# Kernel tuning notes

Measured on AMD Instinct MI355X. Metric: run time of the kernel, lower is better.

The kernel has to match this reference:

```python
import jax, jax.numpy as jnp
import numpy as np

B, N, HID, H, DH, NB = 4, 4096, 768, 12, 64, 266
EPS = 1e-4


def softmax_kernel(data, proj, is_query):
    # data: [B,H,N,DH], proj: [NB,DH]. FAVOR+ positive softmax features.
    d = data.shape[-1]
    ratio = proj.shape[0] ** -0.5
    dn = d ** -0.25  # data normalizer
    data_dash = jnp.einsum('bhnd,jd->bhnj', data * dn, proj)  # [B,H,N,NB]
    diag = 0.5 * jnp.sum((data * dn) ** 2, axis=-1, keepdims=True)  # [B,H,N,1]
    if is_query:
        m = jnp.max(data_dash, axis=-1, keepdims=True)
    else:
        m = jnp.max(data_dash, axis=(-1, -2), keepdims=True)
    return ratio * (jnp.exp(data_dash - diag - m) + EPS)


def setup_inputs() -> dict:
    key = jax.random.key(0)
    ks = jax.random.split(key, 8)
    s = HID ** -0.5
    return {
        'hidden_states': jax.random.normal(ks[0], (B, N, HID), jnp.float32),
        'Wq': jax.random.normal(ks[1], (HID, HID), jnp.float32) * s,
        'bq': jnp.zeros((HID,), jnp.float32),
        'Wk': jax.random.normal(ks[2], (HID, HID), jnp.float32) * s,
        'bk': jnp.zeros((HID,), jnp.float32),
        'Wv': jax.random.normal(ks[3], (HID, HID), jnp.float32) * s,
        'bv': jnp.zeros((HID,), jnp.float32),
        'proj': jax.random.normal(ks[4], (NB, DH), jnp.float32),
    }


def reference(hidden_states, Wq, bq, Wk, bk, Wv, bv, proj):
    def heads(x):  # [B,N,HID] -> [B,H,N,DH]
        return x.reshape(B, N, H, DH).transpose(0, 2, 1, 3)

    q = heads(hidden_states @ Wq.T + bq)
    k = heads(hidden_states @ Wk.T + bk)
    v = heads(hidden_states @ Wv.T + bv)

    qp = softmax_kernel(q, proj, True)   # [B,H,N,NB]
    kp = softmax_kernel(k, proj, False)  # [B,H,N,NB]

    # non-causal linear attention: out = q' (k'^T v) / (q' sum_n k')
    k_sum = jnp.sum(kp, axis=2)                               # [B,H,NB]
    d_inv = 1.0 / jnp.einsum('bhnj,bhj->bhn', qp, k_sum)      # [B,H,N]
    ctx = jnp.einsum('bhnj,bhnd->bhjd', kp, v)                # [B,H,NB,DH]
    out = jnp.einsum('bhnj,bhjd->bhnd', qp, ctx) * d_inv[..., None]

    return out.transpose(0, 2, 1, 3).reshape(B, N, HID)
```

## Files before the change

kernel.cpp:

```cpp
#include <hip/hip_runtime.h>
#include <hip/hip_bf16.h>
#include <stdint.h>

#define B_   4
#define N_   4096
#define HID_ 768
#define H_   12
#define DH_  64
#define NB_  266
#define NBP_ 288
#define EPS_ 1e-4f
#define RATIO_ 0.06131393f

typedef unsigned short u16;
typedef __attribute__((ext_vector_type(8))) short short8;
typedef __attribute__((ext_vector_type(4))) float floatx4;

__device__ __forceinline__ u16 f2b(float f) {
  __hip_bfloat16 h = __float2bfloat16(f);
  return *reinterpret_cast<u16*>(&h);
}
__device__ __forceinline__ float b2f(u16 u) {
  union { unsigned u; float f; } x; x.u = ((unsigned)u) << 16; return x.f;
}
__device__ __forceinline__ unsigned fmap(float x) {
  unsigned u = __float_as_uint(x);
  return (u & 0x80000000u) ? ~u : (u | 0x80000000u);
}
__device__ __forceinline__ float funmap(unsigned u) {
  unsigned b = (u & 0x80000000u) ? (u & 0x7FFFFFFFu) : ~u;
  return __uint_as_float(b);
}
__device__ __forceinline__ void gl16(const u16* g, u16* l) {
  __builtin_amdgcn_global_load_lds(
      (const __attribute__((address_space(1))) void*)g,
      (__attribute__((address_space(3))) void*)l, 16, 0, 0);
}

__global__ __launch_bounds__(256) void k_prep(
    const float4* __restrict__ hs, const float4* __restrict__ Wq,
    const float4* __restrict__ Wk, const float4* __restrict__ Wv,
    const float* __restrict__ proj,
    uint2* __restrict__ hsb, uint2* __restrict__ wb3, u16* __restrict__ projb,
    float* __restrict__ Vdz, unsigned* __restrict__ mbuf) {
  int blk = blockIdx.x;
  const int t = threadIdx.x;
  if (blk < 12288) {
    int i = blk * 256 + t;
    float4 v = hs[i];
    union { u16 s[4]; uint2 u; } pk;
    pk.s[0] = f2b(v.x); pk.s[1] = f2b(v.y); pk.s[2] = f2b(v.z); pk.s[3] = f2b(v.w);
    hsb[i] = pk.u;
    return;
  }
  blk -= 12288;
  if (blk < 1728) {
    int i = blk * 256 + t;
    int sel = i / 147456, j = i - sel * 147456;
    const float4* s = (sel == 0) ? Wq : (sel == 1) ? Wk : Wv;
    float4 v = s[j];
    union { u16 s4[4]; uint2 u; } pk;
    pk.s4[0] = f2b(v.x); pk.s4[1] = f2b(v.y); pk.s4[2] = f2b(v.z); pk.s4[3] = f2b(v.w);
    wb3[i] = pk.u;
    return;
  }
  blk -= 1728;
  if (blk < 72) {
    int i = blk * 256 + t;
    int j = i / DH_, d = i - j * DH_;
    float v = (j < NB_) ? proj[j * DH_ + d] * 0.35355339059327373f : 0.f;
    projb[i] = f2b(v);
    return;
  }
  blk -= 72;
  if (blk < 12) {
    int i = blk * 256 + t;
    Vdz[i] = 0.f;
    return;
  }
  if (t < B_ * H_) mbuf[t] = 0u;
}

__global__ __launch_bounds__(256) void k_qkv3(
    const u16* __restrict__ hsb, const u16* __restrict__ wb,
    const float* __restrict__ bq, const float* __restrict__ bk, const float* __restrict__ bv,
    u16* __restrict__ qb, u16* __restrict__ kb, u16* __restrict__ vT,
    float* __restrict__ diagk, float* __restrict__ Vd) {
  __shared__ u16 lds[3 * 8192];
  const int m0 = blockIdx.x * 128;
  const int bn = blockIdx.y;
  const int sel = bn / 6;
  const int or0 = (bn % 6) * 128;
  const u16* W = wb + (size_t)sel * HID_ * HID_;
  const int t = threadIdx.x, lane = t & 63, wv = t >> 6;
  const int lm = lane & 15, lq = lane >> 4;
  const int wr = (wv >> 1) * 64, wc = (wv & 1) * 64;
  const int srow = t >> 2;
  const int scol = ((t & 3) ^ ((t >> 3) & 3)) * 8;
  const u16* gA0 = hsb + (size_t)(m0 + srow) * HID_ + scol;
  const u16* gB0 = W + (size_t)(or0 + srow) * HID_ + scol;
  u16* lb = lds + wv * 512;
  const int slotc = (lq ^ ((lm >> 1) & 3)) * 8;
  const int aoff = (wr + lm) * 32 + slotc;
  const int boff = 4096 + (wc + lm) * 32 + slotc;

  floatx4 acc[4][4];
#pragma unroll
  for (int mt = 0; mt < 4; mt++)
#pragma unroll
    for (int nt = 0; nt < 4; nt++) acc[mt][nt] = (floatx4){0.f, 0.f, 0.f, 0.f};

#define STAGE_QKV(kt)                                            \
  {                                                              \
    const int k0_ = (kt) * 32;                                   \
    u16* l_ = lb + ((kt) % 3) * 8192;                            \
    gl16(gA0 + k0_, l_);                                         \
    gl16(gA0 + 64 * HID_ + k0_, l_ + 2048);                      \
    gl16(gB0 + k0_, l_ + 4096);                                  \
    gl16(gB0 + 64 * HID_ + k0_, l_ + 6144);                      \
  }

  STAGE_QKV(0);
  STAGE_QKV(1);
  asm volatile("s_waitcnt vmcnt(4)" ::: "memory");
  __builtin_amdgcn_s_barrier();

  for (int kt = 0; kt < 24; ++kt) {
    if (kt + 2 < 24) STAGE_QKV(kt + 2);
    const u16* bufA = lds + (kt % 3) * 8192;
    short8 af[4], bf[4];
#pragma unroll
    for (int mt = 0; mt < 4; mt++) af[mt] = *(const short8*)&bufA[aoff + mt * 512];
#pragma unroll
    for (int nt = 0; nt < 4; nt++) bf[nt] = *(const short8*)&bufA[boff + nt * 512];
    __builtin_amdgcn_s_setprio(1);
#pragma unroll
    for (int mt = 0; mt < 4; mt++)
#pragma unroll
      for (int nt = 0; nt < 4; nt++)
        acc[mt][nt] = __builtin_amdgcn_mfma_f32_16x16x32_bf16(af[mt], bf[nt], acc[mt][nt], 0, 0, 0);
    __builtin_amdgcn_s_setprio(0);
    if (kt < 22) asm volatile("s_waitcnt vmcnt(4)" ::: "memory");
    else         asm volatile("s_waitcnt vmcnt(0)" ::: "memory");
    __builtin_amdgcn_s_barrier();
  }
#undef STAGE_QKV

  if (sel == 0) {
#pragma unroll
    for (int nt = 0; nt < 4; nt++) {
      int lc = or0 + wc + nt * 16 + lm;
      float bb = bq[lc];
#pragma unroll
      for (int mt = 0; mt < 4; mt++) {
        int rowb = m0 + wr + mt * 16 + lq * 4;
#pragma unroll
        for (int r = 0; r < 4; r++)
          qb[(size_t)(rowb + r) * HID_ + lc] = f2b(acc[mt][nt][r] + bb);
      }
    }
  } else if (sel == 1) {
    float dsq[4][4];
#pragma unroll
    for (int mt = 0; mt < 4; mt++)
#pragma unroll
      for (int r = 0; r < 4; r++) dsq[mt][r] = 0.f;
#pragma unroll
    for (int nt = 0; nt < 4; nt++) {
      int lc = or0 + wc + nt * 16 + lm;
      float bb = bk[lc];
#pragma unroll
      for (int mt = 0; mt < 4; mt++) {
        int rowb = m0 + wr + mt * 16 + lq * 4;
#pragma unroll
        for (int r = 0; r < 4; r++) {
          u16 hv = f2b(acc[mt][nt][r] + bb);
          kb[(size_t)(rowb + r) * HID_ + lc] = hv;
          float fv = b2f(hv);
          dsq[mt][r] += fv * fv;
        }
      }
    }
    const int bh0 = (m0 >> 12) * H_ + ((or0 + wc) >> 6);
#pragma unroll
    for (int mt = 0; mt < 4; mt++)
#pragma unroll
      for (int r = 0; r < 4; r++) {
        float v = dsq[mt][r];
        v += __shfl_xor(v, 1); v += __shfl_xor(v, 2);
        v += __shfl_xor(v, 4); v += __shfl_xor(v, 8);
        if (lm == 0) {
          int rowb = m0 + wr + mt * 16 + lq * 4 + r;
          diagk[(size_t)bh0 * N_ + (rowb & 4095)] = 0.0625f * v;
        }
      }
  } else {
    const int hh = (or0 + wc) >> 6;
#pragma unroll
    for (int nt = 0; nt < 4; nt++) {
      int lc = or0 + wc + nt * 16 + lm;
      int dv = nt * 16 + lm;
      float bb = bv[lc];
      float vs = 0.f;
#pragma unroll
      for (int mt = 0; mt < 4; mt++) {
        int rowbase = m0 + wr + mt * 16 + lq * 4;
        int b = rowbase >> 12, n = rowbase & 4095;
        union { u16 s[4]; uint2 u; } pk;
#pragma unroll
        for (int r = 0; r < 4; r++) {
          float fv = acc[mt][nt][r] + bb;
          vs += fv;
          pk.s[r] = f2b(fv);
        }
        *(uint2*)(vT + ((size_t)(b * H_ + hh) * DH_ + dv) * N_ + n) = pk.u;
      }
      vs += __shfl_xor(vs, 16);
      vs += __shfl_xor(vs, 32);
      if (lq == 0) atomicAdd(&Vd[((m0 >> 12) * H_ + hh) * DH_ + dv], vs);
    }
  }
}

__global__ __launch_bounds__(256) void k_ctx5(
    const u16* __restrict__ kb, const u16* __restrict__ vT, const u16* __restrict__ projb,
    const float* __restrict__ diagk,
    float* __restrict__ ksumS, float* __restrict__ ctxTf, unsigned* __restrict__ mbuf) {
  __shared__ u16 kpl[32 * 72];
  __shared__ float kred[4][2][16];
  const int orig = blockIdx.x;
  const int lg = (orig & 7) * 54 + (orig >> 3);
  const int bh = lg / 9, jb = lg - bh * 9;
  const int j0 = jb * 32;
  const int b = bh / H_, h = bh - b * H_;
  const int t = threadIdx.x, lane = t & 63, wv = t >> 6;
  const int lm = lane & 15, lq = lane >> 4;
  const bool vj0 = (j0 + lm) < NB_;
  const bool vj1 = (j0 + 16 + lm) < NB_;
  short8 bp00, bp01, bp10, bp11;
  {
    const u16* pp = projb + (j0 + lm) * DH_ + lq * 8;
    bp00 = *(const short8*)pp;
    bp01 = *(const short8*)(pp + 32);
    pp += 16 * DH_;
    bp10 = *(const short8*)pp;
    bp11 = *(const short8*)(pp + 32);
  }
  const u16* kbB = kb + (size_t)(b * N_) * HID_ + h * DH_;
  const u16* vTb = vT + ((size_t)bh * DH_ + wv * 16 + lm) * N_;
  const float* dgB = diagk + (size_t)bh * N_;
  floatx4 acc0 = (floatx4){0.f,0.f,0.f,0.f}, acc1 = (floatx4){0.f,0.f,0.f,0.f};
  float kacc0 = 0.f, kacc1 = 0.f;
  float am = -3e38f;
  const u16* kr0 = kbB + (size_t)(wv * 16 + lm) * HID_ + lq * 8;
  short8 af0 = *(const short8*)kr0;
  short8 af1 = *(const short8*)(kr0 + 32);
  floatx4 dg4 = *(const floatx4*)(dgB + wv * 16 + lq * 4);

  for (int n64 = 0; n64 < N_; n64 += 64) {
    __syncthreads();
    const int nn = (n64 + 64 < N_) ? n64 + 64 : 0;
    const u16* krn = kbB + (size_t)(nn + wv * 16 + lm) * HID_ + lq * 8;
    short8 nf0 = *(const short8*)krn;
    short8 nf1 = *(const short8*)(krn + 32);
    floatx4 nd = *(const floatx4*)(dgB + nn + wv * 16 + lq * 4);
    short8 av0 = *(const short8*)(vTb + n64 + lq * 8);
    short8 av1 = *(const short8*)(vTb + n64 + 32 + lq * 8);
    {
      floatx4 a = __builtin_amdgcn_mfma_f32_16x16x32_bf16(af0, bp00, (floatx4){0.f,0.f,0.f,0.f}, 0, 0, 0);
      a = __builtin_amdgcn_mfma_f32_16x16x32_bf16(af1, bp01, a, 0, 0, 0);
      union { u16 s[4]; uint2 u; } pk;
      float kss = 0.f;
#pragma unroll
      for (int r = 0; r < 4; r++) {
        float tv = __expf(a[r] - dg4[r]);
        if (vj0) am = fmaxf(am, a[r]);
        kss += tv;
        pk.s[r] = f2b(tv);
      }
      kacc0 += kss;
      *(uint2*)&kpl[lm * 72 + wv * 16 + lq * 4] = pk.u;
      a = __builtin_amdgcn_mfma_f32_16x16x32_bf16(af0, bp10, (floatx4){0.f,0.f,0.f,0.f}, 0, 0, 0);
      a = __builtin_amdgcn_mfma_f32_16x16x32_bf16(af1, bp11, a, 0, 0, 0);
      kss = 0.f;
#pragma unroll
      for (int r = 0; r < 4; r++) {
        float tv = __expf(a[r] - dg4[r]);
        if (vj1) am = fmaxf(am, a[r]);
        kss += tv;
        pk.s[r] = f2b(tv);
      }
      kacc1 += kss;
      *(uint2*)&kpl[(16 + lm) * 72 + wv * 16 + lq * 4] = pk.u;
    }
    __syncthreads();
    {
      short8 bf = *(const short8*)&kpl[lm * 72 + lq * 8];
      acc0 = __builtin_amdgcn_mfma_f32_16x16x32_bf16(av0, bf, acc0, 0, 0, 0);
      bf = *(const short8*)&kpl[(16 + lm) * 72 + lq * 8];
      acc1 = __builtin_amdgcn_mfma_f32_16x16x32_bf16(av0, bf, acc1, 0, 0, 0);
      bf = *(const short8*)&kpl[lm * 72 + 32 + lq * 8];
      acc0 = __builtin_amdgcn_mfma_f32_16x16x32_bf16(av1, bf, acc0, 0, 0, 0);
      bf = *(const short8*)&kpl[(16 + lm) * 72 + 32 + lq * 8];
      acc1 = __builtin_amdgcn_mfma_f32_16x16x32_bf16(av1, bf, acc1, 0, 0, 0);
    }
    af0 = nf0; af1 = nf1; dg4 = nd;
  }
  {
    float v0 = kacc0; v0 += __shfl_xor(v0, 16); v0 += __shfl_xor(v0, 32);
    float v1 = kacc1; v1 += __shfl_xor(v1, 16); v1 += __shfl_xor(v1, 32);
    if (lq == 0) { kred[wv][0][lm] = v0; kred[wv][1][lm] = v1; }
  }
  __syncthreads();
  if (t < 32) {
    int jh = t >> 4, l = t & 15;
    ksumS[bh * NBP_ + j0 + t] =
        kred[0][jh][l] + kred[1][jh][l] + kred[2][jh][l] + kred[3][jh][l];
  }
  {
    float* cb = ctxTf + ((size_t)bh * DH_ + wv * 16 + lq * 4) * NBP_ + j0 + lm;
#pragma unroll
    for (int r = 0; r < 4; r++) {
      cb[(size_t)r * NBP_] = acc0[r];
      cb[(size_t)r * NBP_ + 16] = acc1[r];
    }
  }
#pragma unroll
  for (int o = 1; o < 64; o <<= 1) am = fmaxf(am, __shfl_xor(am, o));
  if (lane == 0) atomicMax(&mbuf[bh], fmap(am));
}

__global__ __launch_bounds__(256) void k_fin(
    const float* __restrict__ ctxTf, const float* __restrict__ ksumS,
    const float* __restrict__ Vd, const unsigned* __restrict__ mbuf,
    u16* __restrict__ ctxb, float* __restrict__ ksumf,
    float* __restrict__ Cc, float* __restrict__ Ck) {
  __shared__ float cks[4];
  const int bh = blockIdx.x;
  const int t = threadIdx.x;
  const float em = __expf(-funmap(mbuf[bh]));
  const int d = t >> 2, q4 = t & 3;
  const float* Tb = ctxTf + ((size_t)bh * DH_ + d) * NBP_;
  u16* cbo = ctxb + ((size_t)bh * DH_ + d) * NBP_;
  const float vd = Vd[bh * DH_ + d];
  float csum = 0.f;
  for (int j = q4 * 72; j < q4 * 72 + 72; j++) {
    float c = (j < NB_) ? RATIO_ * (em * Tb[j] + EPS_ * vd) : 0.f;
    csum += c;
    cbo[j] = f2b(c);
  }
  csum += __shfl_xor(csum, 1);
  csum += __shfl_xor(csum, 2);
  if (q4 == 0) Cc[bh * DH_ + d] = csum;
  float ck = 0.f;
  for (int j = t; j < NBP_; j += 256) {
    float kv = (j < NB_) ? RATIO_ * (em * ksumS[bh * NBP_ + j] + EPS_ * 4096.0f) : 0.f;
    ksumf[bh * NBP_ + j] = kv;
    ck += kv;
  }
#pragma unroll
  for (int o = 1; o < 64; o <<= 1) ck += __shfl_xor(ck, o);
  if ((t & 63) == 0) cks[t >> 6] = ck;
  __syncthreads();
  if (t == 0) Ck[bh] = cks[0] + cks[1] + cks[2] + cks[3];
}

__global__ __launch_bounds__(256) void k_out5(
    const u16* __restrict__ qb, const u16* __restrict__ projb,
    const u16* __restrict__ ctxb, const float* __restrict__ ksumf,
    const float* __restrict__ Cc, const float* __restrict__ Ck,
    float* __restrict__ outp) {
  __shared__ u16 qpl[4][16][296];
  const int bh = blockIdx.y, b = bh / H_, h = bh - b * H_;
  const int t = threadIdx.x, lane = t & 63, wv = t >> 6;
  const int lm = lane & 15, lq = lane >> 4;
  const int row0 = blockIdx.x * 64 + wv * 16;
  const u16* cb = ctxb + (size_t)bh * DH_ * NBP_;
  const float* ksb = ksumf + bh * NBP_;
  float ksv[17];
#pragma unroll
  for (int ct = 0; ct < 17; ct++) ksv[ct] = ksb[ct * 16 + lm];
  const float ckv = Ck[bh];

  const u16* prow = qb + (size_t)(b * N_ + row0 + lm) * HID_ + h * DH_ + lq * 8;
  short8 af0 = *(const short8*)prow;
  short8 af1 = *(const short8*)(prow + 32);
  float rs = 0.f;
#pragma unroll
  for (int i = 0; i < 8; i++) { float f = b2f(((const u16*)&af0)[i]); rs += f * f; }
#pragma unroll
  for (int i = 0; i < 8; i++) { float f = b2f(((const u16*)&af1)[i]); rs += f * f; }
  rs += __shfl_xor(rs, 16);
  rs += __shfl_xor(rs, 32);
  float dg[4];
#pragma unroll
  for (int r = 0; r < 4; r++) dg[r] = 0.0625f * __shfl(rs, lq * 4 + r);

  float tmax[4] = {0.f, 0.f, 0.f, 0.f};
  float skp[4] = {0.f, 0.f, 0.f, 0.f};
#pragma unroll
  for (int ct = 0; ct < 17; ct++) {
    const u16* pp = projb + (ct * 16 + lm) * DH_ + lq * 8;
    short8 bf0 = *(const short8*)pp;
    short8 bf1 = *(const short8*)(pp + 32);
    floatx4 a = __builtin_amdgcn_mfma_f32_16x16x32_bf16(af0, bf0, (floatx4){0.f,0.f,0.f,0.f}, 0, 0, 0);
    a = __builtin_amdgcn_mfma_f32_16x16x32_bf16(af1, bf1, a, 0, 0, 0);
    bool valid = (ct < 16) || (lm < 10);
#pragma unroll
    for (int r = 0; r < 4; r++) {
      float tv = __expf(a[r] - dg[r]);
      if (valid) tmax[r] = fmaxf(tmax[r], tv);
      skp[r] += tv * ksv[ct];
      qpl[wv][lq * 4 + r][ct * 16 + lm] = f2b(tv);
    }
  }
#pragma unroll
  for (int r = 0; r < 4; r++) qpl[wv][lq * 4 + r][272 + lm] = 0;
#pragma unroll
  for (int o = 1; o < 16; o <<= 1) {
#pragma unroll
    for (int r = 0; r < 4; r++) {
      tmax[r] = fmaxf(tmax[r], __shfl_xor(tmax[r], o));
      skp[r] += __shfl_xor(skp[r], o);
    }
  }
  float alpha[4], beta[4];
#pragma unroll
  for (int r = 0; r < 4; r++) {
    float s = __expf(-dg[r]) / tmax[r];
    float dinv = 1.f / (s * skp[r] + EPS_ * ckv);
    alpha[r] = s * dinv;
    beta[r] = EPS_ * dinv;
  }

  floatx4 ao[4];
#pragma unroll
  for (int dt = 0; dt < 4; dt++) ao[dt] = (floatx4){0.f, 0.f, 0.f, 0.f};
#pragma unroll
  for (int ks9 = 0; ks9 < 9; ks9++) {
    short8 aq = *(const short8*)&qpl[wv][lm][ks9 * 32 + lq * 8];
#pragma unroll
    for (int dt = 0; dt < 4; dt++) {
      short8 bc = *(const short8*)(cb + (size_t)(dt * 16 + lm) * NBP_ + ks9 * 32 + lq * 8);
      ao[dt] = __builtin_amdgcn_mfma_f32_16x16x32_bf16(aq, bc, ao[dt], 0, 0, 0);
    }
  }
#pragma unroll
  for (int dt = 0; dt < 4; dt++) {
    float ccd = Cc[bh * DH_ + dt * 16 + lm];
#pragma unroll
    for (int r = 0; r < 4; r++) {
      int n = row0 + lq * 4 + r;
      outp[((size_t)(b * N_ + n)) * HID_ + h * DH_ + dt * 16 + lm] =
          ao[dt][r] * alpha[r] + ccd * beta[r];
    }
  }
}

extern "C" void kernel_launch(void* const* d_in, const int* in_sizes, int n_in,
                              void* d_out, int out_size, void* d_ws, size_t ws_size,
                              hipStream_t stream) {
  (void)in_sizes; (void)n_in; (void)out_size; (void)ws_size;
  const float* hs   = (const float*)d_in[0];
  const float* Wq   = (const float*)d_in[1];
  const float* bq   = (const float*)d_in[2];
  const float* Wk   = (const float*)d_in[3];
  const float* bk   = (const float*)d_in[4];
  const float* Wv   = (const float*)d_in[5];
  const float* bv   = (const float*)d_in[6];
  const float* proj = (const float*)d_in[7];

  char* w = (char*)d_ws;
  u16* hsb   = (u16*)w;  w += (size_t)16384 * 768 * 2;
  u16* wb3   = (u16*)w;  w += (size_t)3 * 768 * 768 * 2;
  u16* projb = (u16*)w;  w += (size_t)NBP_ * 64 * 2;
  u16* qb    = (u16*)w;  w += (size_t)16384 * 768 * 2;
  u16* kb    = (u16*)w;  w += (size_t)16384 * 768 * 2;
  u16* vT    = (u16*)w;  w += (size_t)48 * DH_ * N_ * 2;
  float* ksumS = (float*)w; w += (size_t)48 * NBP_ * 4;
  float* ksumf = (float*)w; w += (size_t)48 * NBP_ * 4;
  float* diagk = (float*)w; w += (size_t)48 * N_ * 4;
  float* ctxTf = (float*)w; w += (size_t)48 * DH_ * NBP_ * 4;
  u16* ctxTb = (u16*)w;  w += (size_t)48 * DH_ * NBP_ * 2;
  float* Vd   = (float*)w; w += (size_t)48 * DH_ * 4;
  float* Cc   = (float*)w; w += (size_t)48 * DH_ * 4;
  float* Ck   = (float*)w; w += (size_t)48 * 4;
  unsigned* mbuf = (unsigned*)w;

  hipLaunchKernelGGL(k_prep, dim3(14101), dim3(256), 0, stream,
                     (const float4*)hs, (const float4*)Wq, (const float4*)Wk, (const float4*)Wv,
                     proj, (uint2*)hsb, (uint2*)wb3, projb, Vd, mbuf);
  hipLaunchKernelGGL(k_qkv3, dim3(128, 18), dim3(256), 0, stream, hsb, wb3, bq, bk, bv, qb, kb, vT, diagk, Vd);
  hipLaunchKernelGGL(k_ctx5, dim3(432), dim3(256), 0, stream, kb, vT, projb, diagk, ksumS, ctxTf, mbuf);
  hipLaunchKernelGGL(k_fin, dim3(48), dim3(256), 0, stream, ctxTf, ksumS, Vd, mbuf, ctxTb, ksumf, Cc, Ck);
  hipLaunchKernelGGL(k_out5, dim3(64, 48), dim3(256), 0, stream, qb, projb, ctxTb, ksumf, Cc, Ck, (float*)d_out);
}
```

Before: 372.5 us.

## Split context reduction over sequence into eight partial slices and parallelize finalize

The context kernel now splits the N=4096 sequence into eight 512-row chunks, launching eight times more blocks (3456 instead of 432). Each block writes partial ctx and k_sum into separate slices. The old single 48-block finalize is replaced by two kernels: one sums the k_sum partials, and a 64x48-block kernel sums the ctx partials and converts them to bf16. This is meant to fill the GPU better, at the cost of extra partial-buffer traffic and one more launch.

```diff
diff --git a/kernel.cpp b/kernel.cpp
--- a/kernel.cpp
+++ b/kernel.cpp
@@ -11,6 +11,8 @@
 #define NBP_ 288
 #define EPS_ 1e-4f
 #define RATIO_ 0.06131393f
+#define CSL_  ((size_t)48 * DH_ * NBP_)
+#define KSL_  ((size_t)48 * NBP_)
 
 typedef unsigned short u16;
 typedef __attribute__((ext_vector_type(8))) short short8;
@@ -222,16 +224,18 @@
   }
 }
 
-__global__ __launch_bounds__(256) void k_ctx5(
+__global__ __launch_bounds__(256) void k_ctx6(
     const u16* __restrict__ kb, const u16* __restrict__ vT, const u16* __restrict__ projb,
     const float* __restrict__ diagk,
-    float* __restrict__ ksumS, float* __restrict__ ctxTf, unsigned* __restrict__ mbuf) {
+    float* __restrict__ ksumS8, float* __restrict__ ctxTf8, unsigned* __restrict__ mbuf) {
   __shared__ u16 kpl[32 * 72];
   __shared__ float kred[4][2][16];
   const int orig = blockIdx.x;
-  const int lg = (orig & 7) * 54 + (orig >> 3);
-  const int bh = lg / 9, jb = lg - bh * 9;
+  const int lg = (orig & 7) * 432 + (orig >> 3);
+  const int bhjb = lg >> 3, ns = lg & 7;
+  const int bh = bhjb / 9, jb = bhjb - bh * 9;
   const int j0 = jb * 32;
+  const int nbeg = ns * 512;
   const int b = bh / H_, h = bh - b * H_;
   const int t = threadIdx.x, lane = t & 63, wv = t >> 6;
   const int lm = lane & 15, lq = lane >> 4;
@@ -252,14 +256,14 @@
   floatx4 acc0 = (floatx4){0.f,0.f,0.f,0.f}, acc1 = (floatx4){0.f,0.f,0.f,0.f};
   float kacc0 = 0.f, kacc1 = 0.f;
   float am = -3e38f;
-  const u16* kr0 = kbB + (size_t)(wv * 16 + lm) * HID_ + lq * 8;
+  const u16* kr0 = kbB + (size_t)(nbeg + wv * 16 + lm) * HID_ + lq * 8;
   short8 af0 = *(const short8*)kr0;
   short8 af1 = *(const short8*)(kr0 + 32);
-  floatx4 dg4 = *(const floatx4*)(dgB + wv * 16 + lq * 4);
-
-  for (int n64 = 0; n64 < N_; n64 += 64) {
+  floatx4 dg4 = *(const floatx4*)(dgB + nbeg + wv * 16 + lq * 4);
+
+  for (int n64 = nbeg; n64 < nbeg + 512; n64 += 64) {
     __syncthreads();
-    const int nn = (n64 + 64 < N_) ? n64 + 64 : 0;
+    const int nn = (n64 + 64 < nbeg + 512) ? n64 + 64 : nbeg;
     const u16* krn = kbB + (size_t)(nn + wv * 16 + lm) * HID_ + lq * 8;
     short8 nf0 = *(const short8*)krn;
     short8 nf1 = *(const short8*)(krn + 32);
@@ -314,11 +318,11 @@
   __syncthreads();
   if (t < 32) {
     int jh = t >> 4, l = t & 15;
-    ksumS[bh * NBP_ + j0 + t] =
+    ksumS8[(size_t)ns * KSL_ + bh * NBP_ + j0 + t] =
         kred[0][jh][l] + kred[1][jh][l] + kred[2][jh][l] + kred[3][jh][l];
   }
   {
-    float* cb = ctxTf + ((size_t)bh * DH_ + wv * 16 + lq * 4) * NBP_ + j0 + lm;
+    float* cb = ctxTf8 + (size_t)ns * CSL_ + ((size_t)bh * DH_ + wv * 16 + lq * 4) * NBP_ + j0 + lm;
 #pragma unroll
     for (int r = 0; r < 4; r++) {
       cb[(size_t)r * NBP_] = acc0[r];
@@ -330,31 +334,20 @@
   if (lane == 0) atomicMax(&mbuf[bh], fmap(am));
 }
 
-__global__ __launch_bounds__(256) void k_fin(
-    const float* __restrict__ ctxTf, const float* __restrict__ ksumS,
-    const float* __restrict__ Vd, const unsigned* __restrict__ mbuf,
-    u16* __restrict__ ctxb, float* __restrict__ ksumf,
-    float* __restrict__ Cc, float* __restrict__ Ck) {
+__global__ __launch_bounds__(256) void k_fink(
+    const float* __restrict__ ksumS8, const unsigned* __restrict__ mbuf,
+    float* __restrict__ ksumf, float* __restrict__ Ck) {
   __shared__ float cks[4];
   const int bh = blockIdx.x;
   const int t = threadIdx.x;
   const float em = __expf(-funmap(mbuf[bh]));
-  const int d = t >> 2, q4 = t & 3;
-  const float* Tb = ctxTf + ((size_t)bh * DH_ + d) * NBP_;
-  u16* cbo = ctxb + ((size_t)bh * DH_ + d) * NBP_;
-  const float vd = Vd[bh * DH_ + d];
-  float csum = 0.f;
-  for (int j = q4 * 72; j < q4 * 72 + 72; j++) {
-    float c = (j < NB_) ? RATIO_ * (em * Tb[j] + EPS_ * vd) : 0.f;
-    csum += c;
-    cbo[j] = f2b(c);
-  }
-  csum += __shfl_xor(csum, 1);
-  csum += __shfl_xor(csum, 2);
-  if (q4 == 0) Cc[bh * DH_ + d] = csum;
   float ck = 0.f;
   for (int j = t; j < NBP_; j += 256) {
-    float kv = (j < NB_) ? RATIO_ * (em * ksumS[bh * NBP_ + j] + EPS_ * 4096.0f) : 0.f;
+    const float* p = ksumS8 + bh * NBP_ + j;
+    float s = p[0];
+#pragma unroll
+    for (int ns = 1; ns < 8; ns++) s += p[(size_t)ns * KSL_];
+    float kv = (j < NB_) ? RATIO_ * (em * s + EPS_ * 4096.0f) : 0.f;
     ksumf[bh * NBP_ + j] = kv;
     ck += kv;
   }
@@ -362,7 +355,34 @@
   for (int o = 1; o < 64; o <<= 1) ck += __shfl_xor(ck, o);
   if ((t & 63) == 0) cks[t >> 6] = ck;
   __syncthreads();
-  if (t == 0) Ck[bh] = cks[0] + cks[1] + cks[2] + cks[3];
+  if (t == 0) Ck[bh] = ((cks[0] + cks[1]) + cks[2]) + cks[3];
+}
+
+__global__ __launch_bounds__(256) void k_finc(
+    const float* __restrict__ ctxTf8, const float* __restrict__ Vd,
+    const unsigned* __restrict__ mbuf,
+    u16* __restrict__ ctxb, float* __restrict__ Cc) {
+  __shared__ float red[4];
+  const int d = blockIdx.x, bh = blockIdx.y;
+  const int t = threadIdx.x;
+  const float em = __expf(-funmap(mbuf[bh]));
+  const float vd = Vd[bh * DH_ + d];
+  const size_t rb = ((size_t)bh * DH_ + d) * NBP_;
+  float csum = 0.f;
+  for (int j = t; j < NBP_; j += 256) {
+    const float* p = ctxTf8 + rb + j;
+    float s = p[0];
+#pragma unroll
+    for (int ns = 1; ns < 8; ns++) s += p[(size_t)ns * CSL_];
+    float c = (j < NB_) ? RATIO_ * (em * s + EPS_ * vd) : 0.f;
+    csum += c;
+    ctxb[rb + j] = f2b(c);
+  }
+#pragma unroll
+  for (int o = 1; o < 64; o <<= 1) csum += __shfl_xor(csum, o);
+  if ((t & 63) == 0) red[t >> 6] = csum;
+  __syncthreads();
+  if (t == 0) Cc[bh * DH_ + d] = ((red[0] + red[1]) + red[2]) + red[3];
 }
 
 __global__ __launch_bounds__(256) void k_out5(
@@ -477,10 +497,10 @@
   u16* qb    = (u16*)w;  w += (size_t)16384 * 768 * 2;
   u16* kb    = (u16*)w;  w += (size_t)16384 * 768 * 2;
   u16* vT    = (u16*)w;  w += (size_t)48 * DH_ * N_ * 2;
-  float* ksumS = (float*)w; w += (size_t)48 * NBP_ * 4;
-  float* ksumf = (float*)w; w += (size_t)48 * NBP_ * 4;
-  float* diagk = (float*)w; w += (size_t)48 * N_ * 4;
-  float* ctxTf = (float*)w; w += (size_t)48 * DH_ * NBP_ * 4;
+  float* ksumS8 = (float*)w; w += (size_t)8 * KSL_ * 4;
+  float* ksumf  = (float*)w; w += (size_t)48 * NBP_ * 4;
+  float* diagk  = (float*)w; w += (size_t)48 * N_ * 4;
+  float* ctxTf8 = (float*)w; w += (size_t)8 * CSL_ * 4;
   u16* ctxTb = (u16*)w;  w += (size_t)48 * DH_ * NBP_ * 2;
   float* Vd   = (float*)w; w += (size_t)48 * DH_ * 4;
   float* Cc   = (float*)w; w += (size_t)48 * DH_ * 4;
@@ -491,7 +511,8 @@
                      (const float4*)hs, (const float4*)Wq, (const float4*)Wk, (const float4*)Wv,
                      proj, (uint2*)hsb, (uint2*)wb3, projb, Vd, mbuf);
   hipLaunchKernelGGL(k_qkv3, dim3(128, 18), dim3(256), 0, stream, hsb, wb3, bq, bk, bv, qb, kb, vT, diagk, Vd);
-  hipLaunchKernelGGL(k_ctx5, dim3(432), dim3(256), 0, stream, kb, vT, projb, diagk, ksumS, ctxTf, mbuf);
-  hipLaunchKernelGGL(k_fin, dim3(48), dim3(256), 0, stream, ctxTf, ksumS, Vd, mbuf, ctxTb, ksumf, Cc, Ck);
+  hipLaunchKernelGGL(k_ctx6, dim3(3456), dim3(256), 0, stream, kb, vT, projb, diagk, ksumS8, ctxTf8, mbuf);
+  hipLaunchKernelGGL(k_fink, dim3(48), dim3(256), 0, stream, ksumS8, mbuf, ksumf, Ck);
+  hipLaunchKernelGGL(k_finc, dim3(64, 48), dim3(256), 0, stream, ctxTf8, Vd, mbuf, ctxTb, Cc);
   hipLaunchKernelGGL(k_out5, dim3(64, 48), dim3(256), 0, stream, qb, projb, ctxTb, ksumf, Cc, Ck, (float*)d_out);
 }
```

After: 377.6 us. No clear change (+1.4%).
